# Optimization experiments

Measured on AMD Instinct MI355X. Metric: run time of the kernel, lower is better.

The kernel has to match this reference:

```python
import jax, jax.numpy as jnp
import numpy as np
import math

N_HEAD = 16
N_CTX = 1024


def setup_inputs() -> dict:
    key = jax.random.key(0)
    ks = jax.random.split(key, 3)
    B, S, NX = 4, 1024, 1024
    x = jax.random.normal(ks[0], (B, S, NX), dtype=jnp.float32)
    # Conv1D weights stored as [nx, nf], init std=0.02, bias zeros
    c_attn_w = jax.random.normal(ks[1], (NX, 3 * NX), dtype=jnp.float32) * 0.02
    c_attn_b = jnp.zeros((3 * NX,), dtype=jnp.float32)
    c_proj_w = jax.random.normal(ks[2], (NX, NX), dtype=jnp.float32) * 0.02
    c_proj_b = jnp.zeros((NX,), dtype=jnp.float32)
    return {"x": x, "c_attn_w": c_attn_w, "c_attn_b": c_attn_b,
            "c_proj_w": c_proj_w, "c_proj_b": c_proj_b}


def reference(x, c_attn_w, c_attn_b, c_proj_w, c_proj_b):
    B, S, NX = x.shape
    H = N_HEAD
    D = NX // H
    # c_attn: Conv1D -> x @ W + b, then split into q, k, v
    qkv = x @ c_attn_w + c_attn_b                      # [B,S,3*NX]
    q, k, v = jnp.split(qkv, 3, axis=-1)               # each [B,S,NX]
    # split heads: q,v -> [B,H,S,D]; k -> [B,H,D,S]
    q = q.reshape(B, S, H, D).transpose(0, 2, 1, 3)
    k = k.reshape(B, S, H, D).transpose(0, 2, 3, 1)
    v = v.reshape(B, S, H, D).transpose(0, 2, 1, 3)
    # _attn: scores, scale, combined multiplicative+additive causal mask, softmax
    w = jnp.matmul(q, k)                               # [B,H,S,S]
    w = w / math.sqrt(D)                               # scale=True
    bias = jnp.tril(jnp.ones((S, S), dtype=w.dtype))[None, None]  # causal tril slice
    w = w * bias - 1e10 * (1.0 - bias)
    w = jax.nn.softmax(w, axis=-1)
    a = jnp.matmul(w, v)                               # [B,H,S,D]
    # merge heads
    a = a.transpose(0, 2, 1, 3).reshape(B, S, NX)
    # c_proj
    return a @ c_proj_w + c_proj_b
```

## Files before the change

kernel.cpp:

```cpp
#include <hip/hip_runtime.h>
#include <cstdint>

typedef __attribute__((ext_vector_type(8))) short short8;
typedef __attribute__((ext_vector_type(4))) short short4x;
typedef __attribute__((ext_vector_type(4))) float floatx4;

__device__ __forceinline__ unsigned short f2b(float f) {
    unsigned int u = __builtin_bit_cast(unsigned int, f);
    u += 0x7fffu + ((u >> 16) & 1u);
    return (unsigned short)(u >> 16);
}
__device__ __forceinline__ float b2f(unsigned short s) {
    unsigned int u = ((unsigned int)s) << 16;
    return __builtin_bit_cast(float, u);
}
__device__ __forceinline__ float fast_exp2(float x) {
    float r;
    asm("v_exp_f32 %0, %1" : "=v"(r) : "v"(x));
    return r;
}
__device__ __forceinline__ unsigned int pack_bf16_trunc(float lo, float hi) {
    return __builtin_amdgcn_perm(__builtin_bit_cast(unsigned int, hi),
                                 __builtin_bit_cast(unsigned int, lo), 0x07060302u);
}

#define GLDS(g, l) __builtin_amdgcn_global_load_lds(                                   \
    (const __attribute__((address_space(1))) unsigned int*)(g),                        \
    (__attribute__((address_space(3))) unsigned int*)(l), 16, 0, 0)

__global__ __launch_bounds__(256) void prep_kernel(const float* __restrict__ x,
                                                   unsigned short* __restrict__ xb,
                                                   const float* __restrict__ w1,
                                                   unsigned short* __restrict__ w1t,
                                                   const float* __restrict__ w2,
                                                   unsigned short* __restrict__ w2t) {
    __shared__ unsigned short tile[64][65];
    const int b = blockIdx.x, t = threadIdx.x;
    if (b < 1024) {
        for (int i = b * 256 + t; i < 1048576; i += 262144) {
            float4 v = ((const float4*)x)[i];
            ushort4 o;
            o.x = f2b(v.x); o.y = f2b(v.y); o.z = f2b(v.z); o.w = f2b(v.w);
            ((ushort4*)xb)[i] = o;
        }
        return;
    }
    const float* W; unsigned short* Wt; int K, N, kb, nb;
    if (b < 1792) { W = w1; Wt = w1t; K = 1024; N = 3072; kb = (b - 1024) & 15; nb = (b - 1024) >> 4; }
    else          { W = w2; Wt = w2t; K = 1024; N = 1024; kb = (b - 1792) & 15; nb = (b - 1792) >> 4; }
    const int k0 = kb * 64, n0 = nb * 64;
    for (int idx = t; idx < 64 * 64; idx += 256) {
        int i = idx >> 6, j = idx & 63;
        tile[j][i] = f2b(W[(size_t)(k0 + i) * N + n0 + j]);
    }
    __syncthreads();
    for (int idx = t; idx < 64 * 64; idx += 256) {
        int r = idx >> 6, c = idx & 63;
        Wt[(size_t)(n0 + r) * K + k0 + c] = tile[r][c];
    }
}

#define MFMA16(a_, b_, c_) __builtin_amdgcn_mfma_f32_16x16x32_bf16((a_), (b_), (c_), 0, 0, 0)

#define GBLDA(mi, kc) (*(const short8*)&As[buf][aRow + (mi) * 1024 + ((kc) ? g1 : g0)])
#define GBLDB(ni, kc) (*(const short8*)&Bs[buf][bRow + (ni) * 1024 + ((kc) ? g1 : g0)])
#define GBSTAGE(kt_) {                                                  \
    const unsigned short* sa_ = aSrc + (kt_) * 64;                      \
    const unsigned short* sb_ = bSrc + (kt_) * 64;                      \
    GLDS(sa_,              &As[(kt_) & 1][ldsOff]);                     \
    GLDS(sa_ + 32 * 1024,  &As[(kt_) & 1][2048 + ldsOff]);              \
    GLDS(sa_ + 64 * 1024,  &As[(kt_) & 1][4096 + ldsOff]);              \
    GLDS(sa_ + 96 * 1024,  &As[(kt_) & 1][6144 + ldsOff]);              \
    GLDS(sb_,              &Bs[(kt_) & 1][ldsOff]);                     \
    GLDS(sb_ + 32 * 1024,  &Bs[(kt_) & 1][2048 + ldsOff]);              \
    GLDS(sb_ + 64 * 1024,  &Bs[(kt_) & 1][4096 + ldsOff]);              \
    GLDS(sb_ + 96 * 1024,  &Bs[(kt_) & 1][6144 + ldsOff]); }

__global__ __launch_bounds__(256) void gemm_bt_kernel(const unsigned short* __restrict__ A,
                                                      const unsigned short* __restrict__ Bt,
                                                      const float* __restrict__ bias,
                                                      unsigned short* __restrict__ C,
                                                      unsigned short* __restrict__ vTout,
                                                      int vSplit) {
    __shared__ unsigned short As[2][128 * 64];
    __shared__ unsigned short Bs[2][128 * 64];

    const int t = threadIdx.x;
    const int wave = t >> 6, lane = t & 63;
    const int quad = lane >> 4, l16 = lane & 15;
    const int rowBase = blockIdx.x << 7;
    const int colBase = blockIdx.y << 7;
    const int waveM = (wave >> 1) * 64;
    const int waveN = (wave & 1) * 64;

    floatx4 acc[4][4];
#pragma unroll
    for (int i = 0; i < 4; ++i)
#pragma unroll
        for (int j = 0; j < 4; ++j) acc[i][j] = (floatx4){0.f, 0.f, 0.f, 0.f};

    const int rr = t >> 3;
    const int gsrc = ((t & 7) ^ (rr & 7)) * 8;
    const unsigned short* aSrc = A + (size_t)(rowBase + rr) * 1024 + gsrc;
    const unsigned short* bSrc = Bt + (size_t)(colBase + rr) * 1024 + gsrc;
    const int ldsOff = t * 8;

    const int rg = l16 & 7;
    const int g0 = (quad ^ rg) * 8;
    const int g1 = g0 ^ 32;
    const int aRow = (waveM + l16) * 64;
    const int bRow = (waveN + l16) * 64;

    GBSTAGE(0);

    for (int kt = 0; kt < 16; ++kt) {
        const int buf = kt & 1;
        asm volatile("s_waitcnt vmcnt(0)" ::: "memory");
        __builtin_amdgcn_s_barrier();
        if (kt + 1 < 16) GBSTAGE(kt + 1);

        short8 af[4][2], bf[4][2];
#pragma unroll
        for (int mi = 0; mi < 4; ++mi) {
            af[mi][0] = GBLDA(mi, 0); af[mi][1] = GBLDA(mi, 1);
        }
#pragma unroll
        for (int ni = 0; ni < 4; ++ni) {
            bf[ni][0] = GBLDB(ni, 0); bf[ni][1] = GBLDB(ni, 1);
        }
        asm volatile("s_waitcnt lgkmcnt(0)" ::: "memory");
        __builtin_amdgcn_sched_barrier(0);
        __builtin_amdgcn_s_setprio(1);
#pragma unroll
        for (int kc = 0; kc < 2; ++kc)
#pragma unroll
            for (int mi = 0; mi < 4; ++mi)
#pragma unroll
                for (int ni = 0; ni < 4; ++ni)
                    acc[mi][ni] = MFMA16(af[mi][kc], bf[ni][kc], acc[mi][ni]);
        __builtin_amdgcn_s_setprio(0);
    }

    if (colBase >= vSplit) {
#pragma unroll
        for (int mi = 0; mi < 4; ++mi)
#pragma unroll
            for (int ni = 0; ni < 4; ++ni) {
                int col = colBase + waveN + ni * 16 + l16 - vSplit;
                float bv = bias[colBase + waveN + ni * 16 + l16];
#pragma unroll
                for (int r = 0; r < 4; ++r) {
                    int row = rowBase + waveM + mi * 16 + quad * 4 + r;
                    vTout[((size_t)((row >> 10) * 16 + (col >> 6)) * 64 + (col & 63)) * 1024
                          + (row & 1023)] = f2b(acc[mi][ni][r] + bv);
                }
            }
    } else {
#pragma unroll
        for (int mi = 0; mi < 4; ++mi)
#pragma unroll
            for (int ni = 0; ni < 4; ++ni) {
                int col = colBase + waveN + ni * 16 + l16;
                float bv = bias[col];
#pragma unroll
                for (int r = 0; r < 4; ++r) {
                    int row = rowBase + waveM + mi * 16 + quad * 4 + r;
                    C[(size_t)row * 3072 + col] = f2b(acc[mi][ni][r] + bv);
                }
            }
    }
}

#define G2LDA(mi, kc) (*(const short8*)&As2[buf][aRow + (mi) * 1024 + ((kc) ? g1 : g0)])
#define G2LDB(ni, kc) (*(const short8*)&Bs2[buf][bRow + (ni) * 1024 + ((kc) ? g1 : g0)])
#define G2STAGE(kt_) { const unsigned short* sa_ = aSrc + (kt_) * 64;   \
    const unsigned short* sb_ = bSrc + (kt_) * 64;                      \
    GLDS(sa_,              &As2[(kt_) & 1][ldsOff]);                    \
    GLDS(sa_ + 64 * 1024,  &As2[(kt_) & 1][4096 + ldsOff]);             \
    GLDS(sb_,              &Bs2[(kt_) & 1][ldsOff]);                    \
    GLDS(sb_ + 64 * 1024,  &Bs2[(kt_) & 1][4096 + ldsOff]); }

__global__ __launch_bounds__(512, 2) void gemm2_kernel(const unsigned short* __restrict__ A,
                                                       const unsigned short* __restrict__ Bt,
                                                       const float* __restrict__ bias,
                                                       float* __restrict__ C) {
    __shared__ unsigned short As2[2][128 * 64];
    __shared__ unsigned short Bs2[2][128 * 64];

    const int t = threadIdx.x;
    const int wave = t >> 6, lane = t & 63;
    const int quad = lane >> 4, l16 = lane & 15;
    const int wm = wave >> 2, wn = wave & 3;
    const int rowBase = blockIdx.x << 7;
    const int colBase = blockIdx.y << 7;

    floatx4 acc[4][2];
#pragma unroll
    for (int i = 0; i < 4; ++i)
#pragma unroll
        for (int j = 0; j < 2; ++j) acc[i][j] = (floatx4){0.f, 0.f, 0.f, 0.f};

    const int rr = t >> 3;
    const int gsrc = ((t & 7) ^ (rr & 7)) * 8;
    const unsigned short* aSrc = A + (size_t)(rowBase + rr) * 1024 + gsrc;
    const unsigned short* bSrc = Bt + (size_t)(colBase + rr) * 1024 + gsrc;
    const int ldsOff = t * 8;

    const int rg = l16 & 7;
    const int g0 = (quad ^ rg) * 8;
    const int g1 = g0 ^ 32;
    const int aRow = (wm * 64 + l16) * 64;
    const int bRow = (wn * 32 + l16) * 64;

    G2STAGE(0);

    for (int kt = 0; kt < 16; ++kt) {
        const int buf = kt & 1;
        asm volatile("s_waitcnt vmcnt(0)" ::: "memory");
        __builtin_amdgcn_s_barrier();
        if (kt + 1 < 16) G2STAGE(kt + 1);

        short8 a0k0 = G2LDA(0, 0), a0k1 = G2LDA(0, 1);
        short8 a1k0 = G2LDA(1, 0), a1k1 = G2LDA(1, 1);
        short8 a2k0 = G2LDA(2, 0), a2k1 = G2LDA(2, 1);
        short8 a3k0 = G2LDA(3, 0), a3k1 = G2LDA(3, 1);
        short8 b0k0 = G2LDB(0, 0), b0k1 = G2LDB(0, 1);
        short8 b1k0 = G2LDB(1, 0), b1k1 = G2LDB(1, 1);
        asm volatile("s_waitcnt lgkmcnt(0)" ::: "memory");
        __builtin_amdgcn_sched_barrier(0);
        __builtin_amdgcn_s_setprio(1);
        acc[0][0] = MFMA16(a0k0, b0k0, acc[0][0]);
        acc[1][0] = MFMA16(a1k0, b0k0, acc[1][0]);
        acc[2][0] = MFMA16(a2k0, b0k0, acc[2][0]);
        acc[3][0] = MFMA16(a3k0, b0k0, acc[3][0]);
        acc[0][1] = MFMA16(a0k0, b1k0, acc[0][1]);
        acc[1][1] = MFMA16(a1k0, b1k0, acc[1][1]);
        acc[2][1] = MFMA16(a2k0, b1k0, acc[2][1]);
        acc[3][1] = MFMA16(a3k0, b1k0, acc[3][1]);
        acc[0][0] = MFMA16(a0k1, b0k1, acc[0][0]);
        acc[1][0] = MFMA16(a1k1, b0k1, acc[1][0]);
        acc[2][0] = MFMA16(a2k1, b0k1, acc[2][0]);
        acc[3][0] = MFMA16(a3k1, b0k1, acc[3][0]);
        acc[0][1] = MFMA16(a0k1, b1k1, acc[0][1]);
        acc[1][1] = MFMA16(a1k1, b1k1, acc[1][1]);
        acc[2][1] = MFMA16(a2k1, b1k1, acc[2][1]);
        acc[3][1] = MFMA16(a3k1, b1k1, acc[3][1]);
        __builtin_amdgcn_s_setprio(0);
    }

#pragma unroll
    for (int mi = 0; mi < 4; ++mi)
#pragma unroll
        for (int ni = 0; ni < 2; ++ni) {
            int col = colBase + wn * 32 + ni * 16 + l16;
            float bv = bias[col];
#pragma unroll
            for (int r = 0; r < 4; ++r) {
                int row = rowBase + wm * 64 + mi * 16 + quad * 4 + r;
                C[(size_t)row * 1024 + col] = acc[mi][ni][r] + bv;
            }
        }
}

__global__ __launch_bounds__(256) void attn_kernel(const unsigned short* __restrict__ qkv,
                                                   const unsigned short* __restrict__ vT,
                                                   unsigned short* __restrict__ aout) {
    __shared__ unsigned short Ks[2][2][4096];
    __shared__ unsigned short Vs[2][2][4096];
    __shared__ unsigned short Tb[4][16 * 72];

    const int p  = blockIdx.x;
    const int bh = blockIdx.y;
    const int b = bh >> 4, h = bh & 15;
    const int qb1 = p, qb2 = 15 - p;
    const int t = threadIdx.x;
    const int wave = t >> 6, lane = t & 63;
    const int quad = lane >> 4, l16 = lane & 15;
    const int h7 = l16 & 7;

    const size_t rowB = (size_t)b * 1024;
    const size_t hoff = (size_t)h * 64;
    const int qA0 = qb1 * 64 + wave * 16;
    const int qB0 = qb2 * 64 + wave * 16;

    const float qscale = 0.125f * 1.44269504f;
    short8 qfA[2], qfB[2];
#pragma unroll
    for (int kc = 0; kc < 2; ++kc) {
        short8 qa = *(const short8*)(qkv + (rowB + qA0 + l16) * 3072 + hoff + kc * 32 + quad * 8);
        short8 qb = *(const short8*)(qkv + (rowB + qB0 + l16) * 3072 + hoff + kc * 32 + quad * 8);
#pragma unroll
        for (int e = 0; e < 8; ++e) {
            qa[e] = (short)f2b(b2f((unsigned short)qa[e]) * qscale);
            qb[e] = (short)f2b(b2f((unsigned short)qb[e]) * qscale);
        }
        qfA[kc] = qa; qfB[kc] = qb;
    }

    const int lr = lane >> 3;
    const int sc8 = (lane & 7) * 8;
    const int gc8 = ((lane & 7) ^ lr) * 8;
    const unsigned short* kSrc = qkv + rowB * 3072 + hoff + 1024;
    const unsigned short* vSrc = vT + (size_t)bh * 65536;

    auto stageT = [&](int kt, int bf, int sl) {
        const unsigned short* kp = kSrc + (size_t)kt * 64 * 3072;
        const unsigned short* vp = vSrc + kt * 64;
        int r0 = wave * 16 + lr, r1 = r0 + 8;
        GLDS(kp + (size_t)r0 * 3072 + gc8, &Ks[bf][sl][r0 * 64 + sc8]);
        GLDS(kp + (size_t)r1 * 3072 + gc8, &Ks[bf][sl][r1 * 64 + sc8]);
        GLDS(vp + (size_t)r0 * 1024 + gc8, &Vs[bf][sl][r0 * 64 + sc8]);
        GLDS(vp + (size_t)r1 * 1024 + gc8, &Vs[bf][sl][r1 * 64 + sc8]);
    };

    float lpA = 0.f, lpB = 0.f;
    floatx4 oA[4], oB[4];
#pragma unroll
    for (int ni = 0; ni < 4; ++ni) {
        oA[ni] = (floatx4){0.f, 0.f, 0.f, 0.f};
        oB[ni] = (floatx4){0.f, 0.f, 0.f, 0.f};
    }

    const int nT = qb2 + 1;
    const int nP = (nT + 1) >> 1;

    auto doTile = [&](int kt, const unsigned short* Kb, const unsigned short* Vb) {
        short8 kf[4][2];
#pragma unroll
        for (int jn = 0; jn < 4; ++jn)
#pragma unroll
            for (int kc = 0; kc < 2; ++kc)
                kf[jn][kc] = *(const short8*)&Kb[(jn * 16 + l16) * 64 + (((kc * 4 + quad) ^ h7) * 8)];
        short4x vf[4][4];
#pragma unroll
        for (int ni = 0; ni < 4; ++ni)
#pragma unroll
            for (int jb = 0; jb < 4; ++jb)
                vf[ni][jb] = *(const short4x*)&Vb[(ni * 16 + l16) * 64 +
                                                 (((jb * 2 + (quad >> 1)) ^ h7) * 8) + (quad & 1) * 4];

        auto qtile = [&](short8 (&qf)[2], floatx4 (&o)[4], float& lp, bool diag) {
            floatx4 s[4];
#pragma unroll
            for (int jn = 0; jn < 4; ++jn) s[jn] = (floatx4){0.f, 0.f, 0.f, 0.f};
#pragma unroll
            for (int jn = 0; jn < 4; ++jn)
#pragma unroll
                for (int kc = 0; kc < 2; ++kc)
                    s[jn] = __builtin_amdgcn_mfma_f32_16x16x32_bf16(kf[jn][kc], qf[kc], s[jn], 0, 0, 0);
            if (diag) {
                int ql = wave * 16 + l16;
#pragma unroll
                for (int jn = 0; jn < 4; ++jn)
#pragma unroll
                    for (int r = 0; r < 4; ++r)
                        if (jn * 16 + quad * 4 + r > ql) s[jn][r] = -1e30f;
            }
            short4x pb[4];
#pragma unroll
            for (int jb = 0; jb < 4; ++jb) {
                float pe0 = fast_exp2(s[jb][0]);
                float pe1 = fast_exp2(s[jb][1]);
                float pe2 = fast_exp2(s[jb][2]);
                float pe3 = fast_exp2(s[jb][3]);
                lp += (pe0 + pe1) + (pe2 + pe3);
                uint2 u;
                u.x = pack_bf16_trunc(pe0, pe1);
                u.y = pack_bf16_trunc(pe2, pe3);
                pb[jb] = __builtin_bit_cast(short4x, u);
            }
#pragma unroll
            for (int jb = 0; jb < 4; ++jb)
#pragma unroll
                for (int ni = 0; ni < 4; ++ni)
                    o[ni] = __builtin_amdgcn_mfma_f32_16x16x16bf16_1k(vf[ni][jb], pb[jb], o[ni], 0, 0, 0);
        };

        qtile(qfB, oB, lpB, kt == qb2);
        if (kt <= qb1) qtile(qfA, oA, lpA, kt == qb1);
    };

    stageT(0, 0, 0);
    stageT(1, 0, 1);

    for (int pi = 0; pi < nP; ++pi) {
        __syncthreads();
        if (pi + 1 < nP) {
            stageT(2 * pi + 2, (pi + 1) & 1, 0);
            if (2 * pi + 3 < nT) stageT(2 * pi + 3, (pi + 1) & 1, 1);
        }
        const int bfI = pi & 1;
        doTile(2 * pi, &Ks[bfI][0][0], &Vs[bfI][0][0]);
        if (2 * pi + 1 < nT) doTile(2 * pi + 1, &Ks[bfI][1][0], &Vs[bfI][1][0]);
    }

    lpA += __shfl_xor(lpA, 16); lpA += __shfl_xor(lpA, 32);
    lpB += __shfl_xor(lpB, 16); lpB += __shfl_xor(lpB, 32);
    const float liA = 1.f / lpA, liB = 1.f / lpB;

    auto writeOut = [&](floatx4 (&o)[4], float li, int q0) {
#pragma unroll
        for (int ni = 0; ni < 4; ++ni)
#pragma unroll
            for (int r = 0; r < 4; ++r)
                Tb[wave][l16 * 72 + ni * 16 + quad * 4 + r] = f2b(o[ni][r] * li);
#pragma unroll
        for (int i = 0; i < 2; ++i) {
            int q = lane >> 2, c = (lane & 3) + 4 * i;
            short8 v = *(const short8*)&Tb[wave][q * 72 + c * 8];
            *(short8*)(aout + (rowB + q0 + q) * 1024 + hoff + c * 8) = v;
        }
    };
    writeOut(oA, liA, qA0);
    writeOut(oB, liB, qB0);
}

extern "C" void kernel_launch(void* const* d_in, const int* in_sizes, int n_in,
                              void* d_out, int out_size, void* d_ws, size_t ws_size,
                              hipStream_t stream) {
    const float* x  = (const float*)d_in[0];
    const float* w1 = (const float*)d_in[1];
    const float* b1 = (const float*)d_in[2];
    const float* w2 = (const float*)d_in[3];
    const float* b2 = (const float*)d_in[4];
    float* out = (float*)d_out;

    unsigned short* xb   = (unsigned short*)d_ws;
    unsigned short* w1t  = xb  + (size_t)4096 * 1024;
    unsigned short* w2t  = w1t + (size_t)3072 * 1024;
    unsigned short* qkv  = w2t + (size_t)1024 * 1024;
    unsigned short* attn = qkv + (size_t)4096 * 3072;
    unsigned short* vTb  = attn + (size_t)4096 * 1024;

    prep_kernel<<<2048, 256, 0, stream>>>(x, xb, w1, w1t, w2, w2t);
    gemm_bt_kernel<<<dim3(32, 24), 256, 0, stream>>>(xb, w1t, b1, qkv, vTb, 2048);
    attn_kernel<<<dim3(8, 64), 256, 0, stream>>>(qkv, vTb, attn);
    gemm2_kernel<<<dim3(32, 8), 512, 0, stream>>>(attn, w2t, b2, out);
}
```

Measured before the change: 174.2 us.

## Switch GEMM to triple-buffered BK=32 pipeline with two stages in flight

Reworks the bf16 GEMM main loop from double-buffered 64-wide K tiles to triple-buffered 32-wide K tiles. Two stages are prefetched, and the wait uses vmcnt(4), so one global-to-LDS load stays outstanding while the current tile is computed. The aim is to hide global load latency better while keeping LDS usage at 48KB. In exchange, the loop runs twice as many iterations and barriers, with half as many MFMAs between each sync.

Result: no change. 175.8 us (+1.0%).

```diff
diff --git a/kernel.cpp b/kernel.cpp
--- a/kernel.cpp
+++ b/kernel.cpp
@@ -62,19 +62,13 @@
 
 #define MFMA16(a_, b_, c_) __builtin_amdgcn_mfma_f32_16x16x32_bf16((a_), (b_), (c_), 0, 0, 0)
 
-#define GBLDA(mi, kc) (*(const short8*)&As[buf][aRow + (mi) * 1024 + ((kc) ? g1 : g0)])
-#define GBLDB(ni, kc) (*(const short8*)&Bs[buf][bRow + (ni) * 1024 + ((kc) ? g1 : g0)])
-#define GBSTAGE(kt_) {                                                  \
-    const unsigned short* sa_ = aSrc + (kt_) * 64;                      \
-    const unsigned short* sb_ = bSrc + (kt_) * 64;                      \
-    GLDS(sa_,              &As[(kt_) & 1][ldsOff]);                     \
-    GLDS(sa_ + 32 * 1024,  &As[(kt_) & 1][2048 + ldsOff]);              \
-    GLDS(sa_ + 64 * 1024,  &As[(kt_) & 1][4096 + ldsOff]);              \
-    GLDS(sa_ + 96 * 1024,  &As[(kt_) & 1][6144 + ldsOff]);              \
-    GLDS(sb_,              &Bs[(kt_) & 1][ldsOff]);                     \
-    GLDS(sb_ + 32 * 1024,  &Bs[(kt_) & 1][2048 + ldsOff]);              \
-    GLDS(sb_ + 64 * 1024,  &Bs[(kt_) & 1][4096 + ldsOff]);              \
-    GLDS(sb_ + 96 * 1024,  &Bs[(kt_) & 1][6144 + ldsOff]); }
+#define GBSTAGE(kt_, bf_) {                                             \
+    const unsigned short* sa_ = aSrc + (kt_) * 32;                      \
+    const unsigned short* sb_ = bSrc + (kt_) * 32;                      \
+    GLDS(sa_,             &As[bf_][ldsOff]);                            \
+    GLDS(sa_ + 64 * 1024, &As[bf_][2048 + ldsOff]);                     \
+    GLDS(sb_,             &Bs[bf_][ldsOff]);                            \
+    GLDS(sb_ + 64 * 1024, &Bs[bf_][2048 + ldsOff]); }
 
 __global__ __launch_bounds__(256) void gemm_bt_kernel(const unsigned short* __restrict__ A,
                                                       const unsigned short* __restrict__ Bt,
@@ -82,8 +76,8 @@
                                                       unsigned short* __restrict__ C,
                                                       unsigned short* __restrict__ vTout,
                                                       int vSplit) {
-    __shared__ unsigned short As[2][128 * 64];
-    __shared__ unsigned short Bs[2][128 * 64];
+    __shared__ unsigned short As[3][128 * 32];
+    __shared__ unsigned short Bs[3][128 * 32];
 
     const int t = threadIdx.x;
     const int wave = t >> 6, lane = t & 63;
@@ -99,46 +93,45 @@
 #pragma unroll
         for (int j = 0; j < 4; ++j) acc[i][j] = (floatx4){0.f, 0.f, 0.f, 0.f};
 
-    const int rr = t >> 3;
-    const int gsrc = ((t & 7) ^ (rr & 7)) * 8;
+    const int rr = t >> 2;
+    const int gsrc = ((t & 3) ^ (rr & 3)) * 8;
     const unsigned short* aSrc = A + (size_t)(rowBase + rr) * 1024 + gsrc;
     const unsigned short* bSrc = Bt + (size_t)(colBase + rr) * 1024 + gsrc;
     const int ldsOff = t * 8;
 
-    const int rg = l16 & 7;
-    const int g0 = (quad ^ rg) * 8;
-    const int g1 = g0 ^ 32;
-    const int aRow = (waveM + l16) * 64;
-    const int bRow = (waveN + l16) * 64;
-
-    GBSTAGE(0);
-
-    for (int kt = 0; kt < 16; ++kt) {
-        const int buf = kt & 1;
-        asm volatile("s_waitcnt vmcnt(0)" ::: "memory");
+    const int g0 = (quad ^ (l16 & 3)) * 8;
+    const int aOff = (waveM + l16) * 32 + g0;
+    const int bOff = (waveN + l16) * 32 + g0;
+
+    GBSTAGE(0, 0);
+    GBSTAGE(1, 1);
+
+    int bufR = 0, bufS = 2;
+    for (int kt = 0; kt < 32; ++kt) {
+        if (kt < 31) asm volatile("s_waitcnt vmcnt(4)" ::: "memory");
+        else         asm volatile("s_waitcnt vmcnt(0)" ::: "memory");
         __builtin_amdgcn_s_barrier();
-        if (kt + 1 < 16) GBSTAGE(kt + 1);
-
-        short8 af[4][2], bf[4][2];
-#pragma unroll
-        for (int mi = 0; mi < 4; ++mi) {
-            af[mi][0] = GBLDA(mi, 0); af[mi][1] = GBLDA(mi, 1);
-        }
-#pragma unroll
-        for (int ni = 0; ni < 4; ++ni) {
-            bf[ni][0] = GBLDB(ni, 0); bf[ni][1] = GBLDB(ni, 1);
-        }
+        if (kt + 2 < 32) GBSTAGE(kt + 2, bufS);
+
+        const unsigned short* Ab = &As[bufR][0];
+        const unsigned short* Bb = &Bs[bufR][0];
+        short8 af[4], bf[4];
+#pragma unroll
+        for (int mi = 0; mi < 4; ++mi) af[mi] = *(const short8*)&Ab[aOff + mi * 512];
+#pragma unroll
+        for (int ni = 0; ni < 4; ++ni) bf[ni] = *(const short8*)&Bb[bOff + ni * 512];
         asm volatile("s_waitcnt lgkmcnt(0)" ::: "memory");
         __builtin_amdgcn_sched_barrier(0);
         __builtin_amdgcn_s_setprio(1);
 #pragma unroll
-        for (int kc = 0; kc < 2; ++kc)
-#pragma unroll
-            for (int mi = 0; mi < 4; ++mi)
-#pragma unroll
-                for (int ni = 0; ni < 4; ++ni)
-                    acc[mi][ni] = MFMA16(af[mi][kc], bf[ni][kc], acc[mi][ni]);
+        for (int mi = 0; mi < 4; ++mi)
+#pragma unroll
+            for (int ni = 0; ni < 4; ++ni)
+                acc[mi][ni] = MFMA16(af[mi], bf[ni], acc[mi][ni]);
         __builtin_amdgcn_s_setprio(0);
+
+        bufR = (bufR == 2) ? 0 : bufR + 1;
+        bufS = (bufS == 2) ? 0 : bufS + 1;
     }
 
     if (colBase >= vSplit) {
```
